# Performance work log

Hardware: AMD Instinct MI355X
Metric: run time of the kernel (lower is better)

The kernel has to match this reference:

```python
import jax, jax.numpy as jnp
import numpy as np

N_NODES = 50000
N_EDGES = 800000
IN_DIM, HID_DIM, OUT_DIM = 768, 512, 256


def setup_inputs() -> dict:
    key = jax.random.key(0)
    k1, k2, k3, k4, k5 = jax.random.split(key, 5)
    x = jax.random.normal(k1, (N_NODES, IN_DIM), dtype=jnp.float32)
    edge_index = jax.random.randint(k2, (2, N_EDGES), 0, N_NODES, dtype=jnp.int64)
    # GCNConv params (glorot-ish init)
    W1 = jax.random.normal(k3, (IN_DIM, HID_DIM), dtype=jnp.float32) / np.sqrt(IN_DIM)
    b1 = jnp.zeros((HID_DIM,), dtype=jnp.float32)
    W2 = jax.random.normal(k4, (HID_DIM, OUT_DIM), dtype=jnp.float32) / np.sqrt(HID_DIM)
    b2 = jnp.zeros((OUT_DIM,), dtype=jnp.float32)
    return {"x": x, "edge_index": edge_index, "W1": W1, "b1": b1, "W2": W2, "b2": b2}


def gcn_conv(x, W, b, src, dst, n_nodes):
    """PyG GCNConv: add self-loops, symmetric degree norm, linear, scatter-add, bias."""
    h = x @ W  # [N, F_out]
    loop = jnp.arange(n_nodes, dtype=src.dtype)
    s = jnp.concatenate([src, loop])  # sources incl. self-loops
    d = jnp.concatenate([dst, loop])  # destinations incl. self-loops
    deg = jax.ops.segment_sum(jnp.ones_like(d, dtype=h.dtype), d, num_segments=n_nodes)
    dinv = jnp.where(deg > 0, jax.lax.rsqrt(deg), 0.0)
    norm = dinv[s] * dinv[d]  # [E+N]
    msgs = h[s] * norm[:, None]  # gather + scale (largest intermediate)
    out = jax.ops.segment_sum(msgs, d, num_segments=n_nodes)  # scatter-add
    return out + b


def reference(x, edge_index, W1, b1, W2, b2):
    src, dst = edge_index[0], edge_index[1]
    n = x.shape[0]
    h = gcn_conv(x, W1, b1, src, dst, n)
    h = jax.nn.relu(h)  # dropout is identity in eval mode
    out = gcn_conv(h, W2, b2, src, dst, n)
    return out
```

## Files before the change

kernel.cpp:

```cpp
#include <hip/hip_runtime.h>

#define N_NODES 50000
#define N_EDGES 800000
#define IN_DIM  768
#define HID_DIM 512
#define OUT_DIM 256
#define M_PAD   50048

typedef __attribute__((ext_vector_type(8))) short shortx8;
typedef __attribute__((ext_vector_type(4))) short shortx4;
typedef __attribute__((ext_vector_type(4))) float floatx4;

#define AS1 __attribute__((address_space(1)))
#define AS3 __attribute__((address_space(3)))

__device__ __forceinline__ unsigned short f2bf_rne(float f) {
    unsigned int u = __float_as_uint(f);
    unsigned int r = u + 0x7FFFu + ((u >> 16) & 1u);
    return (unsigned short)(r >> 16);
}
__device__ __forceinline__ float bf2f(unsigned short h) {
    return __uint_as_float(((unsigned int)h) << 16);
}

__global__ void count_deg_kernel(const int* __restrict__ dst, int* __restrict__ deg,
                                 int n_edges) {
    int e = blockIdx.x * blockDim.x + threadIdx.x;
    if (e < n_edges) atomicAdd(&deg[dst[e]], 1);
}

#define SCAN_B 256
#define N_SCAN_BLOCKS ((N_NODES + SCAN_B - 1) / SCAN_B)

__global__ void block_sum_kernel(const int* __restrict__ deg, int* __restrict__ partials,
                                 int n) {
    __shared__ int sm[SCAN_B];
    int i = blockIdx.x * SCAN_B + threadIdx.x;
    sm[threadIdx.x] = (i < n) ? deg[i] : 0;
    __syncthreads();
    for (int off = SCAN_B / 2; off > 0; off >>= 1) {
        if (threadIdx.x < off) sm[threadIdx.x] += sm[threadIdx.x + off];
        __syncthreads();
    }
    if (threadIdx.x == 0) partials[blockIdx.x] = sm[0];
}

__global__ void scan_partials_kernel(const int* __restrict__ partials,
                                     int* __restrict__ bases, int nb) {
    __shared__ int sm[SCAN_B];
    int v = (threadIdx.x < nb) ? partials[threadIdx.x] : 0;
    sm[threadIdx.x] = v;
    __syncthreads();
    for (int off = 1; off < SCAN_B; off <<= 1) {
        int t = (threadIdx.x >= off) ? sm[threadIdx.x - off] : 0;
        __syncthreads();
        sm[threadIdx.x] += t;
        __syncthreads();
    }
    if (threadIdx.x < nb) bases[threadIdx.x] = sm[threadIdx.x] - v;
}

__global__ void finalize_scan_kernel(const int* __restrict__ deg, const int* __restrict__ bases,
                                     int* __restrict__ offsets, int* __restrict__ cursor,
                                     float* __restrict__ dinv, int n) {
    __shared__ int sm[SCAN_B];
    int i = blockIdx.x * SCAN_B + threadIdx.x;
    int v = (i < n) ? deg[i] : 0;
    sm[threadIdx.x] = v;
    __syncthreads();
    for (int off = 1; off < SCAN_B; off <<= 1) {
        int t = (threadIdx.x >= off) ? sm[threadIdx.x - off] : 0;
        __syncthreads();
        sm[threadIdx.x] += t;
        __syncthreads();
    }
    if (i < n) {
        int incl = bases[blockIdx.x] + sm[threadIdx.x];
        int o = incl - v;
        offsets[i] = o;
        cursor[i]  = o;
        dinv[i]    = rsqrtf((float)(v + 1));
        if (i == n - 1) offsets[n] = incl;
    }
}

__global__ void fill_csr_kernel(const int* __restrict__ src, const int* __restrict__ dst,
                                int* __restrict__ cursor, int* __restrict__ csr_src,
                                int n_edges) {
    int e = blockIdx.x * blockDim.x + threadIdx.x;
    if (e < n_edges) {
        int p = atomicAdd(&cursor[dst[e]], 1);
        csr_src[p] = src[e];
    }
}

__global__ void convert_split_kernel(const float* __restrict__ x,
                                     unsigned short* __restrict__ xhi,
                                     unsigned short* __restrict__ xlo,
                                     long long n4) {
    long long i = (long long)blockIdx.x * blockDim.x + threadIdx.x;
    if (i >= n4) return;
    float4 v = *reinterpret_cast<const float4*>(x + i * 4);
    ushort4 h, l;
    h.x = f2bf_rne(v.x); l.x = f2bf_rne(v.x - bf2f(h.x));
    h.y = f2bf_rne(v.y); l.y = f2bf_rne(v.y - bf2f(h.y));
    h.z = f2bf_rne(v.z); l.z = f2bf_rne(v.z - bf2f(h.z));
    h.w = f2bf_rne(v.w); l.w = f2bf_rne(v.w - bf2f(h.w));
    *reinterpret_cast<ushort4*>(xhi + i * 4) = h;
    *reinterpret_cast<ushort4*>(xlo + i * 4) = l;
}

__global__ void transpose_split_kernel(const float* __restrict__ W,
                                       unsigned short* __restrict__ Whi,
                                       unsigned short* __restrict__ Wlo,
                                       int K, int N) {
    __shared__ float tile[32][33];
    int n0 = blockIdx.x * 32, k0 = blockIdx.y * 32;
    int tx = threadIdx.x, ty = threadIdx.y;
    tile[ty][tx] = W[(size_t)(k0 + ty) * N + n0 + tx];
    __syncthreads();
    float v = tile[tx][ty];
    unsigned short h = f2bf_rne(v);
    size_t o = (size_t)(n0 + ty) * K + k0 + tx;
    Whi[o] = h;
    Wlo[o] = f2bf_rne(v - bf2f(h));
}

#define GBK 32

__global__ __launch_bounds__(256, 4)
void gemm_bf16x3_kernel(const unsigned short* __restrict__ Ahi,
                        const unsigned short* __restrict__ Alo,
                        const unsigned short* __restrict__ Bhi,
                        const unsigned short* __restrict__ Blo,
                        const float* __restrict__ dinv,
                        unsigned short* __restrict__ C,
                        int M, int N, int K) {
    __shared__ __align__(16) unsigned short As[2][128][GBK];
    __shared__ __align__(16) unsigned short Bs[2][128][GBK];

    const int tid  = threadIdx.x;
    const int lane = tid & 63;
    const int wave = tid >> 6;

    const int gx   = gridDim.x;
    const int nwg  = gx * gridDim.y;
    const int blin = blockIdx.y * gx + blockIdx.x;
    const int qq   = nwg >> 3, rr = nwg & 7;
    const int xcd  = blin & 7, idx = blin >> 3;
    const int tt   = (xcd < rr ? xcd * (qq + 1) : rr * (qq + 1) + (xcd - rr) * qq) + idx;
    const int rowBase = (tt / gx) * 128;
    const int colBase = (tt % gx) * 128;

    const unsigned short* gsrc =
        (wave == 0) ? Ahi : (wave == 1) ? Alo : (wave == 2) ? Bhi : Blo;
    unsigned short* lbase =
        (wave == 0) ? &As[0][0][0] : (wave == 1) ? &As[1][0][0]
      : (wave == 2) ? &Bs[0][0][0] : &Bs[1][0][0];
    const int rbase = (wave < 2) ? rowBase : colBase;
    const int cg = ((lane & 3) ^ ((lane >> 3) & 3)) * 8;
    const size_t laneRowOff = (size_t)(rbase + (lane >> 2)) * K + cg;

    const int m0  = (wave & 1) * 64;
    const int n0  = (wave >> 1) * 64;
    const int r16 = lane & 15;
    const int kswz = ((lane >> 4) ^ ((r16 >> 1) & 3)) * 8;

    floatx4 acc[4][4] = {};

    for (int k0 = 0; k0 < K; k0 += GBK) {
#pragma unroll
        for (int j = 0; j < 8; j++) {
            const unsigned short* g = gsrc + laneRowOff + (size_t)(j * 16) * K + k0;
            __builtin_amdgcn_global_load_lds((const AS1 void*)g,
                                             (AS3 void*)(lbase + j * 16 * GBK),
                                             16, 0, 0);
        }
        __syncthreads();

        shortx8 bh[4], bv[4];
#pragma unroll
        for (int j = 0; j < 4; j++) {
            bh[j] = *reinterpret_cast<const shortx8*>(&Bs[0][n0 + j * 16 + r16][kswz]);
            bv[j] = *reinterpret_cast<const shortx8*>(&Bs[1][n0 + j * 16 + r16][kswz]);
        }
#pragma unroll
        for (int i = 0; i < 4; i++) {
            shortx8 ah = *reinterpret_cast<const shortx8*>(&As[0][m0 + i * 16 + r16][kswz]);
            shortx8 al = *reinterpret_cast<const shortx8*>(&As[1][m0 + i * 16 + r16][kswz]);
#pragma unroll
            for (int j = 0; j < 4; j++) {
                acc[i][j] = __builtin_amdgcn_mfma_f32_16x16x32_bf16(ah, bh[j], acc[i][j], 0, 0, 0);
                acc[i][j] = __builtin_amdgcn_mfma_f32_16x16x32_bf16(ah, bv[j], acc[i][j], 0, 0, 0);
                acc[i][j] = __builtin_amdgcn_mfma_f32_16x16x32_bf16(al, bh[j], acc[i][j], 0, 0, 0);
            }
        }
        __syncthreads();
    }

#pragma unroll
    for (int i = 0; i < 4; i++) {
        int rsub = rowBase + m0 + i * 16 + (lane >> 4) * 4;
#pragma unroll
        for (int j = 0; j < 4; j++) {
            int col = colBase + n0 + j * 16 + r16;
#pragma unroll
            for (int r = 0; r < 4; r++) {
                int row = rsub + r;
                if (row < M) C[(size_t)row * N + col] = f2bf_rne(acc[i][j][r] * dinv[row]);
            }
        }
    }
}

__global__ __launch_bounds__(256)
void aggregate1_kernel(const unsigned short* __restrict__ hs, const int* __restrict__ offsets,
                       const int* __restrict__ csr_src, const float* __restrict__ dinv,
                       const float* __restrict__ bias,
                       unsigned short* __restrict__ yhi,
                       unsigned short* __restrict__ ylo) {
    const int wave = threadIdx.x >> 6;
    const int lane = threadIdx.x & 63;
    const int node = blockIdx.x * 4 + wave;
    const int c = lane * 8;
    const unsigned short* hp = hs + c;

    const int beg = offsets[node], end = offsets[node + 1];
    const float dv = dinv[node];
    floatx4 b0 = *reinterpret_cast<const floatx4*>(bias + c);
    floatx4 b1 = *reinterpret_cast<const floatx4*>(bias + c + 4);

    float acc[8];
    {
        shortx8 r = *reinterpret_cast<const shortx8*>(hp + (size_t)node * HID_DIM);
#pragma unroll
        for (int q = 0; q < 8; q++) acc[q] = bf2f((unsigned short)r[q]);
    }

#define A1_SUM8(r0,r1,r2,r3,r4,r5,r6,r7)                                        \
    _Pragma("unroll")                                                            \
    for (int q = 0; q < 8; q++)                                                  \
        acc[q] += ((bf2f((unsigned short)r0[q]) + bf2f((unsigned short)r1[q]))   \
                 + (bf2f((unsigned short)r2[q]) + bf2f((unsigned short)r3[q])))  \
                + ((bf2f((unsigned short)r4[q]) + bf2f((unsigned short)r5[q]))   \
                 + (bf2f((unsigned short)r6[q]) + bf2f((unsigned short)r7[q])));

    for (int base = beg; base < end; base += 64) {
        int cnt = min(64, end - base);
        int myidx = (base + lane < end) ? csr_src[base + lane] : 0;
        int j = 0;
        for (; j + 16 <= cnt; j += 16) {
            shortx8 r0 = *reinterpret_cast<const shortx8*>(hp + (size_t)__shfl(myidx, j + 0) * HID_DIM);
            shortx8 r1 = *reinterpret_cast<const shortx8*>(hp + (size_t)__shfl(myidx, j + 1) * HID_DIM);
            shortx8 r2 = *reinterpret_cast<const shortx8*>(hp + (size_t)__shfl(myidx, j + 2) * HID_DIM);
            shortx8 r3 = *reinterpret_cast<const shortx8*>(hp + (size_t)__shfl(myidx, j + 3) * HID_DIM);
            shortx8 r4 = *reinterpret_cast<const shortx8*>(hp + (size_t)__shfl(myidx, j + 4) * HID_DIM);
            shortx8 r5 = *reinterpret_cast<const shortx8*>(hp + (size_t)__shfl(myidx, j + 5) * HID_DIM);
            shortx8 r6 = *reinterpret_cast<const shortx8*>(hp + (size_t)__shfl(myidx, j + 6) * HID_DIM);
            shortx8 r7 = *reinterpret_cast<const shortx8*>(hp + (size_t)__shfl(myidx, j + 7) * HID_DIM);
            shortx8 r8 = *reinterpret_cast<const shortx8*>(hp + (size_t)__shfl(myidx, j + 8) * HID_DIM);
            shortx8 r9 = *reinterpret_cast<const shortx8*>(hp + (size_t)__shfl(myidx, j + 9) * HID_DIM);
            shortx8 ra = *reinterpret_cast<const shortx8*>(hp + (size_t)__shfl(myidx, j + 10) * HID_DIM);
            shortx8 rb = *reinterpret_cast<const shortx8*>(hp + (size_t)__shfl(myidx, j + 11) * HID_DIM);
            shortx8 rc = *reinterpret_cast<const shortx8*>(hp + (size_t)__shfl(myidx, j + 12) * HID_DIM);
            shortx8 rd = *reinterpret_cast<const shortx8*>(hp + (size_t)__shfl(myidx, j + 13) * HID_DIM);
            shortx8 re = *reinterpret_cast<const shortx8*>(hp + (size_t)__shfl(myidx, j + 14) * HID_DIM);
            shortx8 rf = *reinterpret_cast<const shortx8*>(hp + (size_t)__shfl(myidx, j + 15) * HID_DIM);
            A1_SUM8(r0, r1, r2, r3, r4, r5, r6, r7)
            A1_SUM8(r8, r9, ra, rb, rc, rd, re, rf)
        }
        for (; j + 8 <= cnt; j += 8) {
            shortx8 r0 = *reinterpret_cast<const shortx8*>(hp + (size_t)__shfl(myidx, j + 0) * HID_DIM);
            shortx8 r1 = *reinterpret_cast<const shortx8*>(hp + (size_t)__shfl(myidx, j + 1) * HID_DIM);
            shortx8 r2 = *reinterpret_cast<const shortx8*>(hp + (size_t)__shfl(myidx, j + 2) * HID_DIM);
            shortx8 r3 = *reinterpret_cast<const shortx8*>(hp + (size_t)__shfl(myidx, j + 3) * HID_DIM);
            shortx8 r4 = *reinterpret_cast<const shortx8*>(hp + (size_t)__shfl(myidx, j + 4) * HID_DIM);
            shortx8 r5 = *reinterpret_cast<const shortx8*>(hp + (size_t)__shfl(myidx, j + 5) * HID_DIM);
            shortx8 r6 = *reinterpret_cast<const shortx8*>(hp + (size_t)__shfl(myidx, j + 6) * HID_DIM);
            shortx8 r7 = *reinterpret_cast<const shortx8*>(hp + (size_t)__shfl(myidx, j + 7) * HID_DIM);
            A1_SUM8(r0, r1, r2, r3, r4, r5, r6, r7)
        }
        for (; j < cnt; j++) {
            shortx8 r = *reinterpret_cast<const shortx8*>(hp + (size_t)__shfl(myidx, j) * HID_DIM);
#pragma unroll
            for (int q = 0; q < 8; q++) acc[q] += bf2f((unsigned short)r[q]);
        }
    }
#undef A1_SUM8

    shortx8 h8, l8;
#pragma unroll
    for (int q = 0; q < 8; q++) {
        float bq = (q < 4) ? b0[q] : b1[q - 4];
        float o = fmaxf(acc[q] * dv + bq, 0.f);
        unsigned short h = f2bf_rne(o);
        h8[q] = (short)h;
        l8[q] = (short)f2bf_rne(o - bf2f(h));
    }
    __builtin_nontemporal_store(h8, reinterpret_cast<shortx8*>(yhi + (size_t)node * HID_DIM + c));
    __builtin_nontemporal_store(l8, reinterpret_cast<shortx8*>(ylo + (size_t)node * HID_DIM + c));
}

__global__ __launch_bounds__(256)
void aggregate2_kernel(const unsigned short* __restrict__ hs, const int* __restrict__ offsets,
                       const int* __restrict__ csr_src, const float* __restrict__ dinv,
                       const float* __restrict__ bias, float* __restrict__ out) {
    const int wave = threadIdx.x >> 6;
    const int lane = threadIdx.x & 63;
    const int node = blockIdx.x * 4 + wave;
    const int c = lane * 4;
    const unsigned short* hp = hs + c;

    const int beg = offsets[node], end = offsets[node + 1];
    const float dv = dinv[node];
    floatx4 b = *reinterpret_cast<const floatx4*>(bias + c);

    float acc[4];
    {
        shortx4 r = *reinterpret_cast<const shortx4*>(hp + (size_t)node * OUT_DIM);
#pragma unroll
        for (int q = 0; q < 4; q++) acc[q] = bf2f((unsigned short)r[q]);
    }

#define A2_SUM8(r0,r1,r2,r3,r4,r5,r6,r7)                                        \
    _Pragma("unroll")                                                            \
    for (int q = 0; q < 4; q++)                                                  \
        acc[q] += ((bf2f((unsigned short)r0[q]) + bf2f((unsigned short)r1[q]))   \
                 + (bf2f((unsigned short)r2[q]) + bf2f((unsigned short)r3[q])))  \
                + ((bf2f((unsigned short)r4[q]) + bf2f((unsigned short)r5[q]))   \
                 + (bf2f((unsigned short)r6[q]) + bf2f((unsigned short)r7[q])));

    for (int base = beg; base < end; base += 64) {
        int cnt = min(64, end - base);
        int myidx = (base + lane < end) ? csr_src[base + lane] : 0;
        int j = 0;
        for (; j + 16 <= cnt; j += 16) {
            shortx4 r0 = *reinterpret_cast<const shortx4*>(hp + (size_t)__shfl(myidx, j + 0) * OUT_DIM);
            shortx4 r1 = *reinterpret_cast<const shortx4*>(hp + (size_t)__shfl(myidx, j + 1) * OUT_DIM);
            shortx4 r2 = *reinterpret_cast<const shortx4*>(hp + (size_t)__shfl(myidx, j + 2) * OUT_DIM);
            shortx4 r3 = *reinterpret_cast<const shortx4*>(hp + (size_t)__shfl(myidx, j + 3) * OUT_DIM);
            shortx4 r4 = *reinterpret_cast<const shortx4*>(hp + (size_t)__shfl(myidx, j + 4) * OUT_DIM);
            shortx4 r5 = *reinterpret_cast<const shortx4*>(hp + (size_t)__shfl(myidx, j + 5) * OUT_DIM);
            shortx4 r6 = *reinterpret_cast<const shortx4*>(hp + (size_t)__shfl(myidx, j + 6) * OUT_DIM);
            shortx4 r7 = *reinterpret_cast<const shortx4*>(hp + (size_t)__shfl(myidx, j + 7) * OUT_DIM);
            shortx4 r8 = *reinterpret_cast<const shortx4*>(hp + (size_t)__shfl(myidx, j + 8) * OUT_DIM);
            shortx4 r9 = *reinterpret_cast<const shortx4*>(hp + (size_t)__shfl(myidx, j + 9) * OUT_DIM);
            shortx4 ra = *reinterpret_cast<const shortx4*>(hp + (size_t)__shfl(myidx, j + 10) * OUT_DIM);
            shortx4 rb = *reinterpret_cast<const shortx4*>(hp + (size_t)__shfl(myidx, j + 11) * OUT_DIM);
            shortx4 rc = *reinterpret_cast<const shortx4*>(hp + (size_t)__shfl(myidx, j + 12) * OUT_DIM);
            shortx4 rd = *reinterpret_cast<const shortx4*>(hp + (size_t)__shfl(myidx, j + 13) * OUT_DIM);
            shortx4 re = *reinterpret_cast<const shortx4*>(hp + (size_t)__shfl(myidx, j + 14) * OUT_DIM);
            shortx4 rf = *reinterpret_cast<const shortx4*>(hp + (size_t)__shfl(myidx, j + 15) * OUT_DIM);
            A2_SUM8(r0, r1, r2, r3, r4, r5, r6, r7)
            A2_SUM8(r8, r9, ra, rb, rc, rd, re, rf)
        }
        for (; j + 8 <= cnt; j += 8) {
            shortx4 r0 = *reinterpret_cast<const shortx4*>(hp + (size_t)__shfl(myidx, j + 0) * OUT_DIM);
            shortx4 r1 = *reinterpret_cast<const shortx4*>(hp + (size_t)__shfl(myidx, j + 1) * OUT_DIM);
            shortx4 r2 = *reinterpret_cast<const shortx4*>(hp + (size_t)__shfl(myidx, j + 2) * OUT_DIM);
            shortx4 r3 = *reinterpret_cast<const shortx4*>(hp + (size_t)__shfl(myidx, j + 3) * OUT_DIM);
            shortx4 r4 = *reinterpret_cast<const shortx4*>(hp + (size_t)__shfl(myidx, j + 4) * OUT_DIM);
            shortx4 r5 = *reinterpret_cast<const shortx4*>(hp + (size_t)__shfl(myidx, j + 5) * OUT_DIM);
            shortx4 r6 = *reinterpret_cast<const shortx4*>(hp + (size_t)__shfl(myidx, j + 6) * OUT_DIM);
            shortx4 r7 = *reinterpret_cast<const shortx4*>(hp + (size_t)__shfl(myidx, j + 7) * OUT_DIM);
            A2_SUM8(r0, r1, r2, r3, r4, r5, r6, r7)
        }
        for (; j < cnt; j++) {
            shortx4 r = *reinterpret_cast<const shortx4*>(hp + (size_t)__shfl(myidx, j) * OUT_DIM);
#pragma unroll
            for (int q = 0; q < 4; q++) acc[q] += bf2f((unsigned short)r[q]);
        }
    }
#undef A2_SUM8

    floatx4 o = { acc[0] * dv + b[0], acc[1] * dv + b[1],
                  acc[2] * dv + b[2], acc[3] * dv + b[3] };
    __builtin_nontemporal_store(o, reinterpret_cast<floatx4*>(out + (size_t)node * OUT_DIM + c));
}

extern "C" void kernel_launch(void* const* d_in, const int* in_sizes, int n_in,
                              void* d_out, int out_size, void* d_ws, size_t ws_size,
                              hipStream_t stream) {
    const float* x    = (const float*)d_in[0];
    const int*   edge = (const int*)d_in[1];
    const float* W1   = (const float*)d_in[2];
    const float* b1   = (const float*)d_in[3];
    const float* W2   = (const float*)d_in[4];
    const float* b2   = (const float*)d_in[5];
    float* out = (float*)d_out;

    const int* src = edge;
    const int* dst = edge + N_EDGES;

    char*  ws  = (char*)d_ws;
    size_t off = 0;
    auto alloc = [&](size_t bytes) -> void* {
        void* p = ws + off;
        off += (bytes + 255) & ~(size_t)255;
        return p;
    };
    int*   deg      = (int*)alloc((size_t)N_NODES * 4);
    float* dinv     = (float*)alloc((size_t)N_NODES * 4);
    int*   offsets  = (int*)alloc((size_t)(N_NODES + 1) * 4);
    int*   cursor   = (int*)alloc((size_t)N_NODES * 4);
    int*   csr_src  = (int*)alloc((size_t)N_EDGES * 4);
    int*   partials = (int*)alloc((size_t)N_SCAN_BLOCKS * 4);
    int*   bases    = (int*)alloc((size_t)N_SCAN_BLOCKS * 4);
    unsigned short* xhi   = (unsigned short*)alloc((size_t)M_PAD * IN_DIM * 2);
    unsigned short* xlo   = (unsigned short*)alloc((size_t)M_PAD * IN_DIM * 2);
    unsigned short* w1thi = (unsigned short*)alloc((size_t)HID_DIM * IN_DIM * 2);
    unsigned short* w1tlo = (unsigned short*)alloc((size_t)HID_DIM * IN_DIM * 2);
    unsigned short* w2thi = (unsigned short*)alloc((size_t)OUT_DIM * HID_DIM * 2);
    unsigned short* w2tlo = (unsigned short*)alloc((size_t)OUT_DIM * HID_DIM * 2);
    unsigned short* hs = (unsigned short*)alloc((size_t)N_NODES * HID_DIM * 2);

    unsigned short* y1hi = xhi;
    unsigned short* y1lo = xlo;

    hipMemsetAsync(deg, 0, (size_t)N_NODES * 4, stream);
    count_deg_kernel<<<(N_EDGES + 255) / 256, 256, 0, stream>>>(dst, deg, N_EDGES);
    block_sum_kernel<<<N_SCAN_BLOCKS, SCAN_B, 0, stream>>>(deg, partials, N_NODES);
    scan_partials_kernel<<<1, SCAN_B, 0, stream>>>(partials, bases, N_SCAN_BLOCKS);
    finalize_scan_kernel<<<N_SCAN_BLOCKS, SCAN_B, 0, stream>>>(deg, bases, offsets, cursor,
                                                               dinv, N_NODES);
    fill_csr_kernel<<<(N_EDGES + 255) / 256, 256, 0, stream>>>(src, dst, cursor, csr_src, N_EDGES);

    long long n4x = (long long)N_NODES * IN_DIM / 4;
    convert_split_kernel<<<(int)((n4x + 255) / 256), 256, 0, stream>>>(x, xhi, xlo, n4x);
    transpose_split_kernel<<<dim3(HID_DIM / 32, IN_DIM / 32), dim3(32, 32), 0, stream>>>(
        W1, w1thi, w1tlo, IN_DIM, HID_DIM);
    transpose_split_kernel<<<dim3(OUT_DIM / 32, HID_DIM / 32), dim3(32, 32), 0, stream>>>(
        W2, w2thi, w2tlo, HID_DIM, OUT_DIM);

    gemm_bf16x3_kernel<<<dim3(HID_DIM / 128, M_PAD / 128), 256, 0, stream>>>(
        xhi, xlo, w1thi, w1tlo, dinv, hs, N_NODES, HID_DIM, IN_DIM);
    aggregate1_kernel<<<N_NODES / 4, 256, 0, stream>>>(
        hs, offsets, csr_src, dinv, b1, y1hi, y1lo);

    gemm_bf16x3_kernel<<<dim3(OUT_DIM / 128, M_PAD / 128), 256, 0, stream>>>(
        y1hi, y1lo, w2thi, w2tlo, dinv, hs, N_NODES, OUT_DIM, HID_DIM);
    aggregate2_kernel<<<N_NODES / 4, 256, 0, stream>>>(
        hs, offsets, csr_src, dinv, b2, out);
}
```

Before: 750.6 us.

## Restructure bf16x3 GEMM into single-wave 64x64 tiles without block barriers

Each GEMM workgroup shrinks from four waves on a shared 128x128 tile to one wave on its own 64x64 tile. The wave loads all four A/B hi/lo slices itself through global_load_lds and waits with an explicit vmcnt, so no __syncthreads is needed. The aim is to remove barrier stalls and raise the number of independent workgroups. In exchange, each loaded tile is reused across less output, so L2/global traffic per FLOP roughly doubles. Load latency is also now hidden only by other resident waves rather than within the workgroup.

```diff
diff --git a/kernel.cpp b/kernel.cpp
--- a/kernel.cpp
+++ b/kernel.cpp
@@ -128,7 +128,7 @@
 
 #define GBK 32
 
-__global__ __launch_bounds__(256, 4)
+__global__ __launch_bounds__(64, 4)
 void gemm_bf16x3_kernel(const unsigned short* __restrict__ Ahi,
                         const unsigned short* __restrict__ Alo,
                         const unsigned short* __restrict__ Bhi,
@@ -136,12 +136,10 @@
                         const float* __restrict__ dinv,
                         unsigned short* __restrict__ C,
                         int M, int N, int K) {
-    __shared__ __align__(16) unsigned short As[2][128][GBK];
-    __shared__ __align__(16) unsigned short Bs[2][128][GBK];
-
-    const int tid  = threadIdx.x;
-    const int lane = tid & 63;
-    const int wave = tid >> 6;
+    __shared__ __align__(16) unsigned short As[2][64][GBK];
+    __shared__ __align__(16) unsigned short Bs[2][64][GBK];
+
+    const int lane = threadIdx.x & 63;
 
     const int gx   = gridDim.x;
     const int nwg  = gx * gridDim.y;
@@ -149,45 +147,49 @@
     const int qq   = nwg >> 3, rr = nwg & 7;
     const int xcd  = blin & 7, idx = blin >> 3;
     const int tt   = (xcd < rr ? xcd * (qq + 1) : rr * (qq + 1) + (xcd - rr) * qq) + idx;
-    const int rowBase = (tt / gx) * 128;
-    const int colBase = (tt % gx) * 128;
-
-    const unsigned short* gsrc =
-        (wave == 0) ? Ahi : (wave == 1) ? Alo : (wave == 2) ? Bhi : Blo;
-    unsigned short* lbase =
-        (wave == 0) ? &As[0][0][0] : (wave == 1) ? &As[1][0][0]
-      : (wave == 2) ? &Bs[0][0][0] : &Bs[1][0][0];
-    const int rbase = (wave < 2) ? rowBase : colBase;
-    const int cg = ((lane & 3) ^ ((lane >> 3) & 3)) * 8;
-    const size_t laneRowOff = (size_t)(rbase + (lane >> 2)) * K + cg;
-
-    const int m0  = (wave & 1) * 64;
-    const int n0  = (wave >> 1) * 64;
+    const int rowBase = (tt / gx) * 64;
+    const int colBase = (tt % gx) * 64;
+
+    const int cg   = ((lane & 3) ^ ((lane >> 3) & 3)) * 8;
+    const int srow = lane >> 2;
+    const size_t aOff = (size_t)(rowBase + srow) * K + cg;
+    const size_t bOff = (size_t)(colBase + srow) * K + cg;
+
     const int r16 = lane & 15;
     const int kswz = ((lane >> 4) ^ ((r16 >> 1) & 3)) * 8;
 
     floatx4 acc[4][4] = {};
 
     for (int k0 = 0; k0 < K; k0 += GBK) {
-#pragma unroll
-        for (int j = 0; j < 8; j++) {
-            const unsigned short* g = gsrc + laneRowOff + (size_t)(j * 16) * K + k0;
-            __builtin_amdgcn_global_load_lds((const AS1 void*)g,
-                                             (AS3 void*)(lbase + j * 16 * GBK),
-                                             16, 0, 0);
-        }
-        __syncthreads();
+        __builtin_amdgcn_sched_barrier(0);
+#pragma unroll
+        for (int j = 0; j < 4; j++) {
+            __builtin_amdgcn_global_load_lds(
+                (const AS1 void*)(Ahi + aOff + (size_t)(j * 16) * K + k0),
+                (AS3 void*)(&As[0][j * 16][0]), 16, 0, 0);
+            __builtin_amdgcn_global_load_lds(
+                (const AS1 void*)(Alo + aOff + (size_t)(j * 16) * K + k0),
+                (AS3 void*)(&As[1][j * 16][0]), 16, 0, 0);
+            __builtin_amdgcn_global_load_lds(
+                (const AS1 void*)(Bhi + bOff + (size_t)(j * 16) * K + k0),
+                (AS3 void*)(&Bs[0][j * 16][0]), 16, 0, 0);
+            __builtin_amdgcn_global_load_lds(
+                (const AS1 void*)(Blo + bOff + (size_t)(j * 16) * K + k0),
+                (AS3 void*)(&Bs[1][j * 16][0]), 16, 0, 0);
+        }
+        asm volatile("s_waitcnt vmcnt(0)" ::: "memory");
+        __builtin_amdgcn_sched_barrier(0);
 
         shortx8 bh[4], bv[4];
 #pragma unroll
         for (int j = 0; j < 4; j++) {
-            bh[j] = *reinterpret_cast<const shortx8*>(&Bs[0][n0 + j * 16 + r16][kswz]);
-            bv[j] = *reinterpret_cast<const shortx8*>(&Bs[1][n0 + j * 16 + r16][kswz]);
+            bh[j] = *reinterpret_cast<const shortx8*>(&Bs[0][j * 16 + r16][kswz]);
+            bv[j] = *reinterpret_cast<const shortx8*>(&Bs[1][j * 16 + r16][kswz]);
         }
 #pragma unroll
         for (int i = 0; i < 4; i++) {
-            shortx8 ah = *reinterpret_cast<const shortx8*>(&As[0][m0 + i * 16 + r16][kswz]);
-            shortx8 al = *reinterpret_cast<const shortx8*>(&As[1][m0 + i * 16 + r16][kswz]);
+            shortx8 ah = *reinterpret_cast<const shortx8*>(&As[0][i * 16 + r16][kswz]);
+            shortx8 al = *reinterpret_cast<const shortx8*>(&As[1][i * 16 + r16][kswz]);
 #pragma unroll
             for (int j = 0; j < 4; j++) {
                 acc[i][j] = __builtin_amdgcn_mfma_f32_16x16x32_bf16(ah, bh[j], acc[i][j], 0, 0, 0);
@@ -195,15 +197,14 @@
                 acc[i][j] = __builtin_amdgcn_mfma_f32_16x16x32_bf16(al, bh[j], acc[i][j], 0, 0, 0);
             }
         }
-        __syncthreads();
     }
 
 #pragma unroll
     for (int i = 0; i < 4; i++) {
-        int rsub = rowBase + m0 + i * 16 + (lane >> 4) * 4;
+        int rsub = rowBase + i * 16 + (lane >> 4) * 4;
 #pragma unroll
         for (int j = 0; j < 4; j++) {
-            int col = colBase + n0 + j * 16 + r16;
+            int col = colBase + j * 16 + r16;
 #pragma unroll
             for (int r = 0; r < 4; r++) {
                 int row = rsub + r;
@@ -432,12 +433,12 @@
     transpose_split_kernel<<<dim3(OUT_DIM / 32, HID_DIM / 32), dim3(32, 32), 0, stream>>>(
         W2, w2thi, w2tlo, HID_DIM, OUT_DIM);
 
-    gemm_bf16x3_kernel<<<dim3(HID_DIM / 128, M_PAD / 128), 256, 0, stream>>>(
+    gemm_bf16x3_kernel<<<dim3(HID_DIM / 64, M_PAD / 64), 64, 0, stream>>>(
         xhi, xlo, w1thi, w1tlo, dinv, hs, N_NODES, HID_DIM, IN_DIM);
     aggregate1_kernel<<<N_NODES / 4, 256, 0, stream>>>(
         hs, offsets, csr_src, dinv, b1, y1hi, y1lo);
 
-    gemm_bf16x3_kernel<<<dim3(OUT_DIM / 128, M_PAD / 128), 256, 0, stream>>>(
+    gemm_bf16x3_kernel<<<dim3(OUT_DIM / 64, M_PAD / 64), 64, 0, stream>>>(
         y1hi, y1lo, w2thi, w2tlo, dinv, hs, N_NODES, OUT_DIM, HID_DIM);
     aggregate2_kernel<<<N_NODES / 4, 256, 0, stream>>>(
         hs, offsets, csr_src, dinv, b2, out);
```

New measurement: 809.0 us. 1.08x slower.

## Add 256x128-tile 512-thread GEMM kernel for first GCN layer

Applied to the files above, without the earlier changes.

Introduces a dedicated layer-1 GEMM using 256x128 output tiles, 8 waves per block, double-buffered direct global-to-LDS loads and the same bf16x3 split MFMA scheme. It replaces the 128x128 kernel for the X@W1 product to raise operand reuse per tile and reduce global traffic for the largest GEMM. M_PAD grows so the row count divides by 256, which enlarges padded buffers and adds some wasted rows. Larger LDS footprint and a 2-block occupancy bound may reduce latency hiding.

```diff
diff --git a/kernel.cpp b/kernel.cpp
--- a/kernel.cpp
+++ b/kernel.cpp
@@ -5,7 +5,7 @@
 #define IN_DIM  768
 #define HID_DIM 512
 #define OUT_DIM 256
-#define M_PAD   50048
+#define M_PAD   50176
 
 typedef __attribute__((ext_vector_type(8))) short shortx8;
 typedef __attribute__((ext_vector_type(4))) short shortx4;
@@ -127,6 +127,120 @@
 }
 
 #define GBK 32
+
+__global__ __launch_bounds__(512, 2)
+void gemm1_256x128_kernel(const unsigned short* __restrict__ Ahi,
+                          const unsigned short* __restrict__ Alo,
+                          const unsigned short* __restrict__ Bhi,
+                          const unsigned short* __restrict__ Blo,
+                          const float* __restrict__ dinv,
+                          unsigned short* __restrict__ C,
+                          int M, int N, int K) {
+    __shared__ __align__(16) unsigned short As[2][2][256][GBK];
+    __shared__ __align__(16) unsigned short Bs[2][2][128][GBK];
+
+    const int tid  = threadIdx.x;
+    const int lane = tid & 63;
+    const int wave = tid >> 6;
+    const int wr   = wave >> 1;
+    const int wc   = wave & 1;
+
+    const int gx   = gridDim.x;
+    const int nwg  = gx * gridDim.y;
+    const int blin = blockIdx.y * gx + blockIdx.x;
+    const int qq   = nwg >> 3, rr = nwg & 7;
+    const int xcd  = blin & 7, idx = blin >> 3;
+    const int tt   = (xcd < rr ? xcd * (qq + 1) : rr * (qq + 1) + (xcd - rr) * qq) + idx;
+    const int rowBase = (tt / gx) * 256;
+    const int colBase = (tt % gx) * 128;
+
+    const int slot = tid & 3;
+    const int arow = tid >> 2;
+    const int cg   = (slot ^ ((tid >> 3) & 3)) * 8;
+    const size_t aOff = (size_t)(rowBase + arow) * K + cg;
+    const size_t bOff = (size_t)(colBase + arow) * K + cg;
+
+    const int r16  = lane & 15;
+    const int kswz = ((lane >> 4) ^ ((r16 >> 1) & 3)) * 8;
+    const int m0   = wr * 64;
+    const int n0   = wc * 64;
+
+    floatx4 acc[4][4] = {};
+    const int nt = K / GBK;
+
+    auto STAGE = [&](int t, int buf) {
+        const size_t k0 = (size_t)t * GBK;
+        unsigned short* ah0 = &As[buf][0][0][0] + (size_t)tid * 8;
+        unsigned short* al0 = &As[buf][1][0][0] + (size_t)tid * 8;
+        unsigned short* bh0 = &Bs[buf][0][0][0] + (size_t)tid * 8;
+        unsigned short* bl0 = &Bs[buf][1][0][0] + (size_t)tid * 8;
+        __builtin_amdgcn_global_load_lds((const AS1 void*)(Ahi + aOff + k0),
+                                         (AS3 void*)ah0, 16, 0, 0);
+        __builtin_amdgcn_global_load_lds((const AS1 void*)(Ahi + aOff + (size_t)128 * K + k0),
+                                         (AS3 void*)(ah0 + 128 * GBK), 16, 0, 0);
+        __builtin_amdgcn_global_load_lds((const AS1 void*)(Alo + aOff + k0),
+                                         (AS3 void*)al0, 16, 0, 0);
+        __builtin_amdgcn_global_load_lds((const AS1 void*)(Alo + aOff + (size_t)128 * K + k0),
+                                         (AS3 void*)(al0 + 128 * GBK), 16, 0, 0);
+        __builtin_amdgcn_global_load_lds((const AS1 void*)(Bhi + bOff + k0),
+                                         (AS3 void*)bh0, 16, 0, 0);
+        __builtin_amdgcn_global_load_lds((const AS1 void*)(Blo + bOff + k0),
+                                         (AS3 void*)bl0, 16, 0, 0);
+    };
+
+    STAGE(0, 0);
+    STAGE(1, 1);
+    asm volatile("s_waitcnt vmcnt(6)\n\ts_barrier" ::: "memory");
+    __builtin_amdgcn_sched_barrier(0);
+
+    int cur = 0;
+    for (int t = 0; t < nt; ++t) {
+        shortx8 ah[4], al[4], bh[4], bl[4];
+#pragma unroll
+        for (int i = 0; i < 4; i++) {
+            ah[i] = *reinterpret_cast<const shortx8*>(&As[cur][0][m0 + i * 16 + r16][kswz]);
+            al[i] = *reinterpret_cast<const shortx8*>(&As[cur][1][m0 + i * 16 + r16][kswz]);
+            bh[i] = *reinterpret_cast<const shortx8*>(&Bs[cur][0][n0 + i * 16 + r16][kswz]);
+            bl[i] = *reinterpret_cast<const shortx8*>(&Bs[cur][1][n0 + i * 16 + r16][kswz]);
+        }
+        asm volatile("s_waitcnt lgkmcnt(0)\n\ts_barrier" ::: "memory");
+        __builtin_amdgcn_sched_barrier(0);
+
+        if (t + 2 < nt) STAGE(t + 2, cur);
+
+        __builtin_amdgcn_s_setprio(1);
+#pragma unroll
+        for (int i = 0; i < 4; i++)
+#pragma unroll
+            for (int j = 0; j < 4; j++) {
+                acc[i][j] = __builtin_amdgcn_mfma_f32_16x16x32_bf16(ah[i], bh[j], acc[i][j], 0, 0, 0);
+                acc[i][j] = __builtin_amdgcn_mfma_f32_16x16x32_bf16(ah[i], bl[j], acc[i][j], 0, 0, 0);
+                acc[i][j] = __builtin_amdgcn_mfma_f32_16x16x32_bf16(al[i], bh[j], acc[i][j], 0, 0, 0);
+            }
+        __builtin_amdgcn_s_setprio(0);
+
+        if (t + 1 < nt) {
+            if (t + 2 < nt) asm volatile("s_waitcnt vmcnt(6)\n\ts_barrier" ::: "memory");
+            else            asm volatile("s_waitcnt vmcnt(0)\n\ts_barrier" ::: "memory");
+            __builtin_amdgcn_sched_barrier(0);
+        }
+        cur ^= 1;
+    }
+
+#pragma unroll
+    for (int i = 0; i < 4; i++) {
+        int rsub = rowBase + m0 + i * 16 + (lane >> 4) * 4;
+#pragma unroll
+        for (int j = 0; j < 4; j++) {
+            int col = colBase + n0 + j * 16 + r16;
+#pragma unroll
+            for (int r = 0; r < 4; r++) {
+                int row = rsub + r;
+                if (row < M) C[(size_t)row * N + col] = f2bf_rne(acc[i][j][r] * dinv[row]);
+            }
+        }
+    }
+}
 
 __global__ __launch_bounds__(256, 4)
 void gemm_bf16x3_kernel(const unsigned short* __restrict__ Ahi,
@@ -432,7 +546,7 @@
     transpose_split_kernel<<<dim3(OUT_DIM / 32, HID_DIM / 32), dim3(32, 32), 0, stream>>>(
         W2, w2thi, w2tlo, HID_DIM, OUT_DIM);
 
-    gemm_bf16x3_kernel<<<dim3(HID_DIM / 128, M_PAD / 128), 256, 0, stream>>>(
+    gemm1_256x128_kernel<<<dim3(HID_DIM / 128, M_PAD / 256), 512, 0, stream>>>(
         xhi, xlo, w1thi, w1tlo, dinv, hs, N_NODES, HID_DIM, IN_DIM);
     aggregate1_kernel<<<N_NODES / 4, 256, 0, stream>>>(
         hs, offsets, csr_src, dinv, b1, y1hi, y1lo);
```

Measured after the change: 789.2 us. +5.1%, slower.
